# Kernel optimization log

Measured on AMD Instinct MI355X. Metric: run time of the kernel, lower is better.

## Reference

```python
import jax, jax.numpy as jnp
import numpy as np

FRAME_LEN = 400
HOP = 160
FFT_LEN = 512
PREEMPH = 0.97
MEL_FLOOR = 1.192092955078125e-07


def _hertz_to_mel(freq):
    return 1127.0 * np.log(1.0 + freq / 700.0)


def _mel_filter_bank(num_frequency_bins=256, num_mel_filters=80, min_frequency=20.0,
                     max_frequency=8000.0, sampling_rate=16000):
    mel_min = _hertz_to_mel(min_frequency)
    mel_max = _hertz_to_mel(max_frequency)
    mel_freqs = np.linspace(mel_min, mel_max, num_mel_filters + 2)
    # NOTE: source has filter_freqs = mel_freqs (mel-space, intentional replication of bug)
    filter_freqs = mel_freqs
    fft_bin_width = sampling_rate / (num_frequency_bins * 2)
    fft_freqs = _hertz_to_mel(fft_bin_width * np.arange(num_frequency_bins))
    filter_diff = np.diff(filter_freqs)
    slopes = filter_freqs[None, :] - fft_freqs[:, None]          # [256, 82]
    down_slopes = -slopes[:, :-2] / filter_diff[:-1]
    up_slopes = slopes[:, 2:] / filter_diff[1:]
    fb = np.maximum(0.0, np.minimum(down_slopes, up_slopes))      # [256, 80]
    # F.pad(mel_filters, (0,0,0,1)) -> one extra zero row -> [257, 80]
    return np.pad(fb, ((0, 1), (0, 0))).astype(np.float32)


def _window():
    n = np.arange(FRAME_LEN)
    hann = 0.5 - 0.5 * np.cos(2.0 * np.pi * n / (FRAME_LEN - 1))  # periodic=False
    return (hann ** 0.85).astype(np.float32)


def setup_inputs() -> dict:
    key = jax.random.key(0)
    T = 9_600_000  # 10 min @ 16 kHz
    raw_speech = jax.random.normal(key, (1, T), dtype=jnp.float32)
    return {
        "raw_speech": raw_speech,
        "mel_filters": jnp.asarray(_mel_filter_bank()),  # [257, 80]
        "window": jnp.asarray(_window()),                # [400]
    }


def reference(raw_speech, mel_filters, window):
    wav = raw_speech.reshape(-1) * 32768.0  # * 2**15
    num_frames = 1 + (wav.shape[0] - FRAME_LEN) // HOP
    idx = jnp.arange(num_frames)[:, None] * HOP + jnp.arange(FRAME_LEN)[None, :]
    frames = wav[idx]                                         # [F, 400]
    frames = frames - frames.mean(axis=1, keepdims=True)      # remove DC offset
    # preemphasis: y[0] = x[0]*(1-p), y[n] = x[n] - p*x[n-1]
    pre = jnp.concatenate(
        [frames[:, :1] * (1.0 - PREEMPH), frames[:, 1:] - PREEMPH * frames[:, :-1]],
        axis=1,
    )
    pre = pre * window
    padded = jnp.pad(pre, ((0, 0), (0, FFT_LEN - FRAME_LEN)))  # [F, 512]
    spec = jnp.abs(jnp.fft.rfft(padded, axis=1)) ** 2          # [F, 257]
    mel = jnp.log(jnp.maximum(spec @ mel_filters, MEL_FLOOR))  # [F, 80]
    mean = mel.mean(axis=0, keepdims=True)
    var = mel.var(axis=0, keepdims=True, ddof=1)               # unbiased
    return (mel - mean) / jnp.sqrt(var + 1e-7)
```

## Files before the change

kernel.cpp:

```cpp
#include <hip/hip_runtime.h>
#include <math.h>

#define FRAME_LEN 400
#define HOP 160
#define NMEL 80
#define PREEMPH 0.97f
#define MEL_FLOOR 1.192092955078125e-07f
#define PPW 4
#define NSHADOW 8

#ifndef __has_builtin
#define __has_builtin(x) 0
#endif
#if __has_builtin(__builtin_amdgcn_permlane16_swap) && __has_builtin(__builtin_amdgcn_permlane32_swap)
#define USE_PLSWAP 1
#else
#define USE_PLSWAP 0
#endif

__device__ __forceinline__ float2 cadd(float2 a, float2 b){ return make_float2(a.x+b.x, a.y+b.y); }
__device__ __forceinline__ float2 csub(float2 a, float2 b){ return make_float2(a.x-b.x, a.y-b.y); }
__device__ __forceinline__ float2 cmul(float2 a, float2 b){ return make_float2(a.x*b.x-a.y*b.y, a.x*b.y+a.y*b.x); }

__device__ __forceinline__ float bperm(int addr, float v) {
    return __int_as_float(__builtin_amdgcn_ds_bpermute(addr, __float_as_int(v)));
}
template<int C>
__device__ __forceinline__ float dppf(float v) {
    return __int_as_float(__builtin_amdgcn_update_dpp(0, __float_as_int(v), C, 0xF, 0xF, false));
}
__device__ __forceinline__ float wscan_add(float v) {
    v += __int_as_float(__builtin_amdgcn_update_dpp(0, __float_as_int(v), 0x111, 0xF, 0xF, false));
    v += __int_as_float(__builtin_amdgcn_update_dpp(0, __float_as_int(v), 0x112, 0xF, 0xF, false));
    v += __int_as_float(__builtin_amdgcn_update_dpp(0, __float_as_int(v), 0x114, 0xF, 0xF, false));
    v += __int_as_float(__builtin_amdgcn_update_dpp(0, __float_as_int(v), 0x118, 0xF, 0xF, false));
    v += __int_as_float(__builtin_amdgcn_update_dpp(0, __float_as_int(v), 0x142, 0xA, 0xF, false));
    v += __int_as_float(__builtin_amdgcn_update_dpp(0, __float_as_int(v), 0x143, 0xC, 0xF, false));
    return v;
}

#if USE_PLSWAP
typedef unsigned int uint2v __attribute__((ext_vector_type(2)));
__device__ __forceinline__ void bflytw16(float2& A, float2& B, float2 tw) {
    uint2v sx = __builtin_amdgcn_permlane16_swap(__float_as_uint(A.x), __float_as_uint(B.x), false, false);
    uint2v sy = __builtin_amdgcn_permlane16_swap(__float_as_uint(A.y), __float_as_uint(B.y), false, false);
    float lx = __uint_as_float(sx.x), hx = __uint_as_float(sx.y);
    float ly = __uint_as_float(sy.x), hy = __uint_as_float(sy.y);
    float cr = tw.x * hx - tw.y * hy;
    float ci = tw.x * hy + tw.y * hx;
    float r1x = lx + cr, r2x = lx - cr;
    float r1y = ly + ci, r2y = ly - ci;
    uint2v tx = __builtin_amdgcn_permlane16_swap(__float_as_uint(r1x), __float_as_uint(r2x), false, false);
    uint2v ty = __builtin_amdgcn_permlane16_swap(__float_as_uint(r1y), __float_as_uint(r2y), false, false);
    A = make_float2(__uint_as_float(tx.x), __uint_as_float(ty.x));
    B = make_float2(__uint_as_float(tx.y), __uint_as_float(ty.y));
}
__device__ __forceinline__ void bflytw32(float2& A, float2& B, float2 tw) {
    uint2v sx = __builtin_amdgcn_permlane32_swap(__float_as_uint(A.x), __float_as_uint(B.x), false, false);
    uint2v sy = __builtin_amdgcn_permlane32_swap(__float_as_uint(A.y), __float_as_uint(B.y), false, false);
    float lx = __uint_as_float(sx.x), hx = __uint_as_float(sx.y);
    float ly = __uint_as_float(sy.x), hy = __uint_as_float(sy.y);
    float cr = tw.x * hx - tw.y * hy;
    float ci = tw.x * hy + tw.y * hx;
    float r1x = lx + cr, r2x = lx - cr;
    float r1y = ly + ci, r2y = ly - ci;
    uint2v tx = __builtin_amdgcn_permlane32_swap(__float_as_uint(r1x), __float_as_uint(r2x), false, false);
    uint2v ty = __builtin_amdgcn_permlane32_swap(__float_as_uint(r1y), __float_as_uint(r2y), false, false);
    A = make_float2(__uint_as_float(tx.x), __uint_as_float(ty.x));
    B = make_float2(__uint_as_float(tx.y), __uint_as_float(ty.y));
}
#endif

__global__ __launch_bounds__(256) void setup_kernel(const float* __restrict__ window,
                                                    float* __restrict__ frtab,
                                                    int* __restrict__ kstab,
                                                    float* __restrict__ wftab)
{
    const int bid = blockIdx.x;
    const int t = threadIdx.x;
    if (bid == 0) {
        __shared__ float uu[256];
        const double mel_min = 1127.0 * log(1.0 + 20.0 / 700.0);
        const double mel_max = 1127.0 * log(1.0 + 8000.0 / 700.0);
        const double dstep = (mel_max - mel_min) / 81.0;
        {
            double fhz = 31.25 * (double)t;
            double m = 1127.0 * log(1.0 + fhz / 700.0);
            uu[t] = (float)((m - mel_min) / dstep);
        }
        __syncthreads();
        {
            float u = uu[t];
            frtab[t] = u - floorf(u);
        }
        if (t < 82) {
            double fhz = 700.0 * (exp((mel_min + (double)t * dstep) / 1127.0) - 1.0);
            int k = (int)ceil(fhz / 31.25);
            k = max(0, min(256, k));
            while (k > 0 && uu[k - 1] >= (float)t) --k;
            while (k < 256 && uu[k] < (float)t) ++k;
            kstab[t] = k;
        }
    } else {
        if (t >= 64) return;
        const int k = bid - 1;
        float sr = 0.f, si = 0.f;
        #pragma unroll
        for (int j = 0; j < 7; ++j) {
            int n = t + 64 * j;
            if (n < FRAME_LEN) {
                float wv = window[n] * 32768.f;
                int m = (k * n) & 511;
                float ang = -3.1415926535897932f * (float)m * (1.0f / 256.0f);
                float sv, cv;
                sincosf(ang, &sv, &cv);
                sr = fmaf(wv, cv, sr);
                si = fmaf(wv, sv, si);
            }
        }
        sr = wscan_add(sr);
        si = wscan_add(si);
        if (t == 63) { wftab[2 * k] = sr; wftab[2 * k + 1] = si; }
    }
}

__global__ __launch_bounds__(64) void feat_kernel(
    const float* __restrict__ raw, const float* __restrict__ window,
    float* __restrict__ mel_out, double* __restrict__ accum,
    const float* __restrict__ frtab, const int* __restrict__ kstab,
    const float* __restrict__ wftab, int F)
{
    __shared__ __align__(16) float wlds[FRAME_LEN];
    __shared__ __align__(16) float xu[560];
    __shared__ __align__(16) float pfx[2][256];

    const int l = threadIdx.x;

    for (int i = l; i < FRAME_LEN; i += 64) wlds[i] = window[i] * 32768.f;

    const int bl   = __brev((unsigned)l) >> 26;
    const int adrX = (l ^ 63) << 2;
    const int adr0 = ((64 - l) & 63) << 2;

#if USE_PLSWAP
    float2 dt[3];
    float  sg[4];
    #pragma unroll
    for (int j = 0; j < 4; ++j) {
        int d = 1 << j;
        sg[j] = (l & d) ? -1.f : 1.f;
        if (j >= 1) {
            float2 tw = make_float2(1.f, 0.f);
            if (l & d) {
                float tt = (float)(l & (d - 1));
                float ang = -3.1415926535897932f * tt / (float)d;
                sincosf(ang, &tw.y, &tw.x);
            }
            dt[j - 1] = tw;
        }
    }
    float2 tw16, tw32;
    {
        float a16 = -3.1415926535897932f * (float)(l & 15) * (1.0f / 16.0f);
        float a32 = -3.1415926535897932f * (float)(l & 31) * (1.0f / 32.0f);
        sincosf(a16, &tw16.y, &tw16.x);
        sincosf(a32, &tw32.y, &tw32.x);
    }
#else
    float2 dt[5];
    float  sg[6];
    #pragma unroll
    for (int j = 0; j < 6; ++j) {
        int d = 1 << j;
        sg[j] = (l & d) ? -1.f : 1.f;
        if (j >= 1) {
            float2 tw = make_float2(1.f, 0.f);
            if (l & d) {
                float tt = (float)(l & (d - 1));
                float ang = -3.1415926535897932f * tt / (float)d;
                sincosf(ang, &tw.y, &tw.x);
            }
            dt[j - 1] = tw;
        }
    }
#endif
    float2 w2[4];
    #pragma unroll
    for (int q = 1; q < 4; ++q) {
        float ang = -6.283185307179586f * (float)(bl * q) * (1.0f / 256.0f);
        sincosf(ang, &w2[q].y, &w2[q].x);
    }
    float2 wk[4];
    #pragma unroll
    for (int q = 0; q < 4; ++q) {
        int k = 4 * l + q;
        float ang = -3.1415926535897932f * (float)k * (1.0f / 256.0f);
        sincosf(ang, &wk[q].y, &wk[q].x);
    }

    float fr1[4];
    {
        float4 fv = *(const float4*)(frtab + 4 * l);
        fr1[0] = fv.x; fr1[1] = fv.y; fr1[2] = fv.z; fr1[3] = fv.w;
    }
    int a0 = kstab[l], b0 = kstab[l + 1], e0 = kstab[l + 2];
    int a1 = 1, b1 = 1, e1 = 1;
    if (l < 16) { a1 = kstab[64 + l]; b1 = kstab[65 + l]; e1 = kstab[66 + l]; }

    const int NP = (F + 1) >> 1;
    const int basePair = blockIdx.x * PPW;

    float acc_s0 = 0.f, acc_q0 = 0.f;
    float acc_s1 = 0.f, acc_q1 = 0.f;

    for (int fi = 0; fi < PPW; ++fi) {
        int P = basePair + fi;
        if (P >= NP) break;
        int fA = 2 * P;
        bool hasB = (fA + 1) < F;

        const float4* g4 = (const float4*)(raw + (size_t)fA * HOP);
        float4 a = g4[l];
        float4 b = make_float4(0.f, 0.f, 0.f, 0.f);
        float4 c = make_float4(0.f, 0.f, 0.f, 0.f);
        if (hasB || l < 36) b = g4[64 + l];
        if (hasB && l < 12) c = g4[128 + l];
        ((float4*)xu)[l] = a;
        ((float4*)xu)[64 + l] = b;
        if (l < 12) ((float4*)xu)[128 + l] = c;

        float as = a.x + a.y + a.z + a.w;
        float bs = b.x + b.y + b.z + b.w;
        float cs = c.x + c.y + c.z + c.w;
        float sA8 = as + (l < 36 ? bs : 0.f);
        float sB8 = (l >= 40 ? as : 0.f) + bs + cs;
        float totA = __int_as_float(__builtin_amdgcn_readlane(__float_as_int(wscan_add(sA8)), 63));
        float totB = __int_as_float(__builtin_amdgcn_readlane(__float_as_int(wscan_add(sB8)), 63));
        float KA = totA * (1.0f / (float)FRAME_LEN) * (1.0f - PREEMPH);
        float KB = totB * (1.0f / (float)FRAME_LEN) * (1.0f - PREEMPH);

        float2 Z[2][4];
        #pragma unroll
        for (int r = 0; r < 4; ++r) {
            int off = 128 * r + 2 * bl;
            if (off < FRAME_LEN) {
                float2 xA = *(const float2*)(xu + off);
                float2 xB = *(const float2*)(xu + 160 + off);
                float xm1A = (off == 0) ? xA.x : xu[off - 1];
                float xm1B = (off == 0) ? xB.x : xu[159 + off];
                float2 wn  = *(const float2*)(wlds + off);
                Z[0][r] = make_float2(fmaf(-PREEMPH, xm1A, xA.x) * wn.x,
                                      fmaf(-PREEMPH, xA.x,  xA.y) * wn.y);
                Z[1][r] = make_float2(fmaf(-PREEMPH, xm1B, xB.x) * wn.x,
                                      fmaf(-PREEMPH, xB.x,  xB.y) * wn.y);
            } else {
                Z[0][r] = make_float2(0.f, 0.f);
                Z[1][r] = make_float2(0.f, 0.f);
            }
        }

        #pragma unroll
        for (int s = 0; s < 2; ++s) {
            float2 t0 = cadd(Z[s][0], Z[s][2]);
            float2 t1 = csub(Z[s][0], Z[s][2]);
            float2 t2 = cadd(Z[s][1], Z[s][3]);
            float2 t3 = csub(Z[s][1], Z[s][3]);
            Z[s][0] = cadd(t0, t2);
            Z[s][2] = csub(t0, t2);
            Z[s][1] = make_float2(t1.x + t3.y, t1.y - t3.x);
            Z[s][3] = make_float2(t1.x - t3.y, t1.y + t3.x);
            #pragma unroll
            for (int q = 1; q < 4; ++q) Z[s][q] = cmul(Z[s][q], w2[q]);
        }

        #pragma unroll
        for (int s = 0; s < 2; ++s)
        #pragma unroll
        for (int q = 0; q < 4; ++q) {
            float ox = dppf<0xB1>(Z[s][q].x), oy = dppf<0xB1>(Z[s][q].y);
            Z[s][q].x = fmaf(sg[0], Z[s][q].x, ox);
            Z[s][q].y = fmaf(sg[0], Z[s][q].y, oy);
        }
        #pragma unroll
        for (int s = 0; s < 2; ++s)
        #pragma unroll
        for (int q = 0; q < 4; ++q) {
            float2 Zw = cmul(Z[s][q], dt[0]);
            float ox = dppf<0x4E>(Zw.x), oy = dppf<0x4E>(Zw.y);
            Z[s][q].x = fmaf(sg[1], Zw.x, ox);
            Z[s][q].y = fmaf(sg[1], Zw.y, oy);
        }
        #pragma unroll
        for (int s = 0; s < 2; ++s)
        #pragma unroll
        for (int q = 0; q < 4; ++q) {
            float2 Zw = cmul(Z[s][q], dt[1]);
            float ox = __shfl_xor(Zw.x, 4, 64), oy = __shfl_xor(Zw.y, 4, 64);
            Z[s][q].x = fmaf(sg[2], Zw.x, ox);
            Z[s][q].y = fmaf(sg[2], Zw.y, oy);
        }
        #pragma unroll
        for (int s = 0; s < 2; ++s)
        #pragma unroll
        for (int q = 0; q < 4; ++q) {
            float2 Zw = cmul(Z[s][q], dt[2]);
            float ox = dppf<0x128>(Zw.x), oy = dppf<0x128>(Zw.y);
            Z[s][q].x = fmaf(sg[3], Zw.x, ox);
            Z[s][q].y = fmaf(sg[3], Zw.y, oy);
        }
#if USE_PLSWAP
        #pragma unroll
        for (int s = 0; s < 2; ++s) {
            bflytw16(Z[s][0], Z[s][1], tw16);
            bflytw16(Z[s][2], Z[s][3], tw16);
        }
        #pragma unroll
        for (int s = 0; s < 2; ++s) {
            bflytw32(Z[s][0], Z[s][1], tw32);
            bflytw32(Z[s][2], Z[s][3], tw32);
        }
#else
        #pragma unroll
        for (int s = 0; s < 2; ++s)
        #pragma unroll
        for (int q = 0; q < 4; ++q) {
            float2 Zw = cmul(Z[s][q], dt[3]);
            float ox = __shfl_xor(Zw.x, 16, 64), oy = __shfl_xor(Zw.y, 16, 64);
            Z[s][q].x = fmaf(sg[4], Zw.x, ox);
            Z[s][q].y = fmaf(sg[4], Zw.y, oy);
        }
        #pragma unroll
        for (int s = 0; s < 2; ++s)
        #pragma unroll
        for (int q = 0; q < 4; ++q) {
            float2 Zw = cmul(Z[s][q], dt[4]);
            float ox = __shfl_xor(Zw.x, 32, 64), oy = __shfl_xor(Zw.y, 32, 64);
            Z[s][q].x = fmaf(sg[5], Zw.x, ox);
            Z[s][q].y = fmaf(sg[5], Zw.y, oy);
        }
#endif

        float4 wfa = ((const float4*)wftab)[2 * l];
        float4 wfb = ((const float4*)wftab)[2 * l + 1];
        float wfr[4] = { wfa.x, wfa.z, wfb.x, wfb.z };
        float wfi[4] = { wfa.y, wfa.w, wfb.y, wfb.w };

        #pragma unroll
        for (int s = 0; s < 2; ++s) {
            float Ks = (s == 0) ? KA : KB;
            float zcr[4], zci[4];
            zcr[0] = bperm(adr0, Z[s][0].x);
            zci[0] = bperm(adr0, Z[s][0].y);
            zcr[1] = bperm(adrX, Z[s][3].x);
            zci[1] = bperm(adrX, Z[s][3].y);
            zcr[2] = bperm(adrX, Z[s][2].x);
            zci[2] = bperm(adrX, Z[s][2].y);
            zcr[3] = bperm(adrX, Z[s][1].x);
            zci[3] = bperm(adrX, Z[s][1].y);

            float pw[4], pv[4];
            #pragma unroll
            for (int q = 0; q < 4; ++q) {
                float Er = 0.5f * (Z[s][q].x + zcr[q]);
                float Ei = 0.5f * (Z[s][q].y - zci[q]);
                float Or = 0.5f * (Z[s][q].y + zci[q]);
                float Oi = 0.5f * (zcr[q] - Z[s][q].x);
                float Xr = Er + Or * wk[q].x - Oi * wk[q].y;
                float Xi = Ei + Or * wk[q].y + Oi * wk[q].x;
                Xr = fmaf(-Ks, wfr[q], Xr);
                Xi = fmaf(-Ks, wfi[q], Xi);
                pw[q] = Xr * Xr + Xi * Xi;
                pv[q] = pw[q] * fr1[q];
            }
            float A0 = pw[0], A1 = A0 + pw[1], A2 = A1 + pw[2], A3 = A2 + pw[3];
            float B0 = pv[0], B1 = B0 + pv[1], B2 = B1 + pv[2], B3 = B2 + pv[3];
            float sA = wscan_add(A3);
            float sB = wscan_add(B3);
            float exA = sA - A3;
            float exB = sB - B3;
            float* pP = pfx[0];
            float* pF = pfx[1];
            ((float4*)pP)[l] = make_float4(exA + A0, exA + A1, exA + A2, exA + A3);
            ((float4*)pF)[l] = make_float4(exB + B0, exB + B1, exB + B2, exB + B3);

            int f = fA + s;
            bool act = (s == 0) || hasB;
            if (act) {
                float E1a = pF[a0 - 1], E1b = pF[b0 - 1], E1e = pF[e0 - 1];
                float EAb = pP[b0 - 1], EAe = pP[e0 - 1];
                float acc = fmaf(2.f, E1b, -E1a) - E1e + (EAe - EAb);
                float v = __logf(fmaxf(acc, MEL_FLOOR));
                mel_out[(size_t)f * NMEL + l] = v;
                acc_s0 += v; acc_q0 = fmaf(v, v, acc_q0);
                if (l < 16) {
                    float F1a = pF[a1 - 1], F1b = pF[b1 - 1], F1e = pF[e1 - 1];
                    float FAb = pP[b1 - 1], FAe = pP[e1 - 1];
                    float ac2 = fmaf(2.f, F1b, -F1a) - F1e + (FAe - FAb);
                    float v1 = __logf(fmaxf(ac2, MEL_FLOOR));
                    mel_out[(size_t)f * NMEL + 64 + l] = v1;
                    acc_s1 += v1; acc_q1 = fmaf(v1, v1, acc_q1);
                }
            }
        }
    }

    double* A = accum + (blockIdx.x & (NSHADOW - 1)) * 160;
    atomicAdd(&A[l], (double)acc_s0);
    atomicAdd(&A[80 + l], (double)acc_q0);
    if (l < 16) {
        atomicAdd(&A[64 + l], (double)acc_s1);
        atomicAdd(&A[144 + l], (double)acc_q1);
    }
}

__global__ __launch_bounds__(256) void norm_kernel(
    float* __restrict__ mel, const double* __restrict__ accum, int F)
{
    __shared__ float s_mean[NMEL], s_inv[NMEL];
    int t = threadIdx.x;
    if (t < NMEL) {
        double S = 0.0, Q = 0.0;
        #pragma unroll
        for (int j = 0; j < NSHADOW; ++j) {
            S += accum[j * 160 + t];
            Q += accum[j * 160 + 80 + t];
        }
        double mean = S / (double)F;
        double var = (Q - S * S / (double)F) / (double)(F - 1);
        s_mean[t] = (float)mean;
        s_inv[t]  = (float)(1.0 / sqrt(var + 1e-7));
    }
    __syncthreads();
    unsigned n = (unsigned)F * NMEL;
    unsigned stride = gridDim.x * 256u * 4u;
    unsigned i = (blockIdx.x * 256u + (unsigned)t) * 4u;
    int c = (int)(i % NMEL);
    float m0 = s_mean[c],     r0 = s_inv[c];
    float m1 = s_mean[c + 1], r1 = s_inv[c + 1];
    float m2 = s_mean[c + 2], r2 = s_inv[c + 2];
    float m3 = s_mean[c + 3], r3 = s_inv[c + 3];
    for (; i < n; i += stride) {
        float4 v = *(float4*)(mel + i);
        v.x = (v.x - m0) * r0;
        v.y = (v.y - m1) * r1;
        v.z = (v.z - m2) * r2;
        v.w = (v.w - m3) * r3;
        *(float4*)(mel + i) = v;
    }
}

extern "C" void kernel_launch(void* const* d_in, const int* in_sizes, int n_in,
                              void* d_out, int out_size, void* d_ws, size_t ws_size,
                              hipStream_t stream)
{
    const float* raw = (const float*)d_in[0];
    const float* window = (const float*)d_in[2];
    float* out = (float*)d_out;

    int N = in_sizes[0];
    int F = 1 + (N - FRAME_LEN) / HOP;

    double* accum = (double*)d_ws;
    float*  frtab = (float*)((char*)d_ws + NSHADOW * 160 * sizeof(double));
    int*    kstab = (int*)((char*)d_ws + 11264);
    float*  wftab = (float*)((char*)d_ws + 11776);

    hipMemsetAsync(d_ws, 0, NSHADOW * 160 * sizeof(double), stream);
    setup_kernel<<<257, 256, 0, stream>>>(window, frtab, kstab, wftab);
    int NP = (F + 1) / 2;
    int gridA = (NP + PPW - 1) / PPW;
    feat_kernel<<<gridA, 64, 0, stream>>>(raw, window, out, accum, frtab, kstab, wftab, F);
    norm_kernel<<<2560, 256, 0, stream>>>(out, accum, F);
}
```

Measured before the change: 141.4 us.

## Prefetch next frame pair into double-buffered LDS and hoist twiddle table load

Adds software pipelining to the per-block frame loop. The global loads for the next frame pair are issued into registers before the current pair's FFT, and they are written into a second LDS buffer after the current buffer has been read, which aims to hide global memory latency behind compute. The wftab twiddle load also moves out of the loop and is done once per thread. In exchange the kernel holds more live registers and uses more LDS, which may lower occupancy in a 64-thread block kernel that relies on many resident waves.

```diff
diff --git a/kernel.cpp b/kernel.cpp
--- a/kernel.cpp
+++ b/kernel.cpp
@@ -131,7 +131,7 @@
     const float* __restrict__ wftab, int F)
 {
     __shared__ __align__(16) float wlds[FRAME_LEN];
-    __shared__ __align__(16) float xu[560];
+    __shared__ __align__(16) float xu[2][560];
     __shared__ __align__(16) float pfx[2][256];
 
     const int l = threadIdx.x;
@@ -198,6 +198,14 @@
         sincosf(ang, &wk[q].y, &wk[q].x);
     }
 
+    float wfr[4], wfi[4];
+    {
+        float4 wfa = ((const float4*)wftab)[2 * l];
+        float4 wfb = ((const float4*)wftab)[2 * l + 1];
+        wfr[0] = wfa.x; wfi[0] = wfa.y; wfr[1] = wfa.z; wfi[1] = wfa.w;
+        wfr[2] = wfb.x; wfi[2] = wfb.y; wfr[3] = wfb.z; wfi[3] = wfb.w;
+    }
+
     float fr1[4];
     {
         float4 fv = *(const float4*)(frtab + 4 * l);
@@ -212,22 +220,41 @@
 
     float acc_s0 = 0.f, acc_q0 = 0.f;
     float acc_s1 = 0.f, acc_q1 = 0.f;
+
+    float4 a = make_float4(0.f,0.f,0.f,0.f);
+    float4 b = make_float4(0.f,0.f,0.f,0.f);
+    float4 c = make_float4(0.f,0.f,0.f,0.f);
+    if (basePair < NP) {
+        int fA0 = 2 * basePair;
+        bool hasB0 = (fA0 + 1) < F;
+        const float4* g4 = (const float4*)(raw + (size_t)fA0 * HOP);
+        a = g4[l];
+        if (hasB0 || l < 36) b = g4[64 + l];
+        if (hasB0 && l < 12) c = g4[128 + l];
+        ((float4*)xu[0])[l] = a;
+        ((float4*)xu[0])[64 + l] = b;
+        if (l < 12) ((float4*)xu[0])[128 + l] = c;
+    }
 
     for (int fi = 0; fi < PPW; ++fi) {
         int P = basePair + fi;
         if (P >= NP) break;
         int fA = 2 * P;
         bool hasB = (fA + 1) < F;
-
-        const float4* g4 = (const float4*)(raw + (size_t)fA * HOP);
-        float4 a = g4[l];
-        float4 b = make_float4(0.f, 0.f, 0.f, 0.f);
-        float4 c = make_float4(0.f, 0.f, 0.f, 0.f);
-        if (hasB || l < 36) b = g4[64 + l];
-        if (hasB && l < 12) c = g4[128 + l];
-        ((float4*)xu)[l] = a;
-        ((float4*)xu)[64 + l] = b;
-        if (l < 12) ((float4*)xu)[128 + l] = c;
+        const int cur = fi & 1;
+
+        float4 a2 = make_float4(0.f,0.f,0.f,0.f);
+        float4 b2 = make_float4(0.f,0.f,0.f,0.f);
+        float4 c2 = make_float4(0.f,0.f,0.f,0.f);
+        const bool ldn = (fi + 1 < PPW) && (P + 1 < NP);
+        if (ldn) {
+            int fAn = 2 * (P + 1);
+            bool hasBn = (fAn + 1) < F;
+            const float4* g4n = (const float4*)(raw + (size_t)fAn * HOP);
+            a2 = g4n[l];
+            if (hasBn || l < 36) b2 = g4n[64 + l];
+            if (hasBn && l < 12) c2 = g4n[128 + l];
+        }
 
         float as = a.x + a.y + a.z + a.w;
         float bs = b.x + b.y + b.z + b.w;
@@ -239,15 +266,16 @@
         float KA = totA * (1.0f / (float)FRAME_LEN) * (1.0f - PREEMPH);
         float KB = totB * (1.0f / (float)FRAME_LEN) * (1.0f - PREEMPH);
 
+        const float* xc = xu[cur];
         float2 Z[2][4];
         #pragma unroll
         for (int r = 0; r < 4; ++r) {
             int off = 128 * r + 2 * bl;
             if (off < FRAME_LEN) {
-                float2 xA = *(const float2*)(xu + off);
-                float2 xB = *(const float2*)(xu + 160 + off);
-                float xm1A = (off == 0) ? xA.x : xu[off - 1];
-                float xm1B = (off == 0) ? xB.x : xu[159 + off];
+                float2 xA = *(const float2*)(xc + off);
+                float2 xB = *(const float2*)(xc + 160 + off);
+                float xm1A = (off == 0) ? xA.x : xc[off - 1];
+                float xm1B = (off == 0) ? xB.x : xc[159 + off];
                 float2 wn  = *(const float2*)(wlds + off);
                 Z[0][r] = make_float2(fmaf(-PREEMPH, xm1A, xA.x) * wn.x,
                                       fmaf(-PREEMPH, xA.x,  xA.y) * wn.y);
@@ -257,6 +285,13 @@
                 Z[0][r] = make_float2(0.f, 0.f);
                 Z[1][r] = make_float2(0.f, 0.f);
             }
+        }
+
+        if (ldn) {
+            float* xn = xu[cur ^ 1];
+            ((float4*)xn)[l] = a2;
+            ((float4*)xn)[64 + l] = b2;
+            if (l < 12) ((float4*)xn)[128 + l] = c2;
         }
 
         #pragma unroll
@@ -339,11 +374,6 @@
             Z[s][q].y = fmaf(sg[5], Zw.y, oy);
         }
 #endif
-
-        float4 wfa = ((const float4*)wftab)[2 * l];
-        float4 wfb = ((const float4*)wftab)[2 * l + 1];
-        float wfr[4] = { wfa.x, wfa.z, wfb.x, wfb.z };
-        float wfi[4] = { wfa.y, wfa.w, wfb.y, wfb.w };
 
         #pragma unroll
         for (int s = 0; s < 2; ++s) {
@@ -402,6 +432,8 @@
                 }
             }
         }
+
+        a = a2; b = b2; c = c2;
     }
 
     double* A = accum + (blockIdx.x & (NSHADOW - 1)) * 160;
```

New measurement: 145.2 us. 2.7% more time.
